# Kernel tuning notes

Hardware: AMD Instinct MI355X
Metric: run time of the kernel (lower is better)

The kernel has to match this reference:

```python
import jax, jax.numpy as jnp
import numpy as np

GROUPS = [16, 16, 32, 64, 192]
B, H, W = 8, 64, 64


def _shift(x, dy, dx):
    # out[i, j] = x[i - dy, j - dx], zero padded (equiv. of PoolConv's depthwise shift convs)
    Hh, Ww = x.shape[-2], x.shape[-1]
    pt, pb = max(dy, 0), max(-dy, 0)
    pl, pr = max(dx, 0), max(-dx, 0)
    xp = jnp.pad(x, ((0, 0), (0, 0), (pt, pb), (pl, pr)))
    return xp[..., pb:pb + Hh, pr:pr + Ww]


def _conv5(x, w, b):
    out = jax.lax.conv_general_dilated(x, w, (1, 1), ((2, 2), (2, 2)),
                                       dimension_numbers=("NCHW", "OIHW", "NCHW"))
    return out + b[None, :, None, None]


def _fill_pool(x, m1):
    # bottom: w[0,0]=1, pad 1 -> shift down-right; top: w[2,0]=1 -> shift up-right; right: w[2,0] of 5x5, pad 2 -> shift right by 2
    xm = x * m1
    return x + _shift(xm, 1, 1) + _shift(xm, -1, 1) + _shift(xm, 0, 2)


def _forward(y, mask, sws, sbs, cws, cbs):
    m0, m1 = mask[0], mask[1]
    starts = np.cumsum([0] + GROUPS[:-1])
    outs = []
    prev = None
    for i, g in enumerate(GROUPS):
        s = y[:, int(starts[i]):int(starts[i]) + g]
        anchor = _fill_pool(s * m0, m1)
        sp = _conv5(anchor, sws[i], sbs[i]) * (1.0 - m0)
        if i == 0:
            outs.append(sp)
            prev = s
        else:
            ch = _conv5(prev, cws[i - 1], cbs[i - 1])
            outs.append(sp)
            outs.append(ch)
            prev = jnp.concatenate([prev, s], axis=1)
    return tuple(outs)


def setup_inputs() -> dict:
    key = jax.random.key(0)
    ks = jax.random.split(key, 32)
    y = jax.random.normal(ks[0], (B, sum(GROUPS), H, W), jnp.float32)
    hh, ww = jnp.meshgrid(jnp.arange(H), jnp.arange(W), indexing="ij")
    m0 = (((hh + ww) % 2) == 0).astype(jnp.float32)[None, None]  # checkerboard anchor mask
    mask = jnp.stack([m0, 1.0 - m0], axis=0)  # [2,1,1,H,W]
    starts = np.cumsum([0] + GROUPS[:-1])
    inp = {"y": y, "mask": mask, "stage": 1}
    for i, g in enumerate(GROUPS):
        inp[f"sw{i}"] = 0.02 * jax.random.normal(ks[1 + i], (2 * g, g, 5, 5), jnp.float32)
        inp[f"sb{i}"] = jnp.zeros((2 * g,), jnp.float32)
    for i in range(1, len(GROUPS)):
        inp[f"cw{i}"] = 0.02 * jax.random.normal(ks[10 + i], (2 * GROUPS[i], int(starts[i]), 5, 5), jnp.float32)
        inp[f"cb{i}"] = jnp.zeros((2 * GROUPS[i],), jnp.float32)
    return inp


def reference(y, mask, stage, sw0, sb0, sw1, sb1, sw2, sb2, sw3, sb3, sw4, sb4,
              cw1, cb1, cw2, cb2, cw3, cb3, cw4, cb4):
    # stage != TRAIN branch: AdaptiveContext returns only the conv output
    return _forward(y, mask,
                    [sw0, sw1, sw2, sw3, sw4], [sb0, sb1, sb2, sb3, sb4],
                    [cw1, cw2, cw3, cw4], [cb1, cb2, cb3, cb4])
```

## Files before the change

kernel.cpp:

```cpp
#include <hip/hip_runtime.h>

typedef __bf16 bf16_t;
typedef __bf16 bf16x8 __attribute__((ext_vector_type(8)));
typedef float f32x16 __attribute__((ext_vector_type(16)));
typedef unsigned int u32;

#define CTOT 320
#define NPIX 32768

__device__ __forceinline__ void gload16(const void* g, void* l) {
  __builtin_amdgcn_global_load_lds((const __attribute__((address_space(1))) u32*)g,
                                   (__attribute__((address_space(3))) u32*)l, 16, 0, 0);
}

__device__ __forceinline__ void sync_drain(bool wait) {
  if (wait) asm volatile("s_waitcnt vmcnt(0)" ::: "memory");
  __builtin_amdgcn_sched_barrier(0);
  __builtin_amdgcn_s_barrier();
  __builtin_amdgcn_sched_barrier(0);
}

struct PrepParams {
  const float* y;
  bf16_t *yt, *ytp, *wt;
  const float* w[9];
  int IC[9], OC[9], OCp[9], wtoff[9], jst[9];
  uint4* zp;
};

__global__ __launch_bounds__(256) void k_prep(PrepParams Q) {
  int blk = blockIdx.x, tid = threadIdx.x;
  if (blk >= 2560) {
    int wb = blk - 2560;
    if (wb >= 572) { if (tid < 64) Q.zp[tid] = uint4{0u, 0u, 0u, 0u}; return; }
    int ci = 0;
#pragma unroll
    for (int i = 1; i < 9; ++i) if (wb >= Q.jst[i]) ci = i;
    int IC = Q.IC[ci], OCp = Q.OCp[ci], OC = Q.OC[ci];
    int idx = (wb - Q.jst[ci]) * 256 + tid;
    if (idx >= OCp * IC) return;
    int oc = idx / IC, ic = idx - oc * IC;
    bool valid = (oc < OC);
    const float* src = Q.w[ci] + (size_t)(oc * IC + ic) * 25;
    bf16_t* dst = Q.wt + Q.wtoff[ci];
    int icg = ic >> 3, ie = ic & 7;
#pragma unroll
    for (int t = 0; t < 25; ++t) {
      float v = valid ? src[t] : 0.0f;
      dst[(size_t)((t * (IC >> 3) + icg) * OCp + oc) * 8 + ie] = (bf16_t)v;
    }
    return;
  }
  __shared__ bf16_t T[64][72];
  int c0 = (blk % 5) * 64;
  int bh = blk / 5;
  int b = bh >> 6, h = bh & 63;
  {
    int c = tid >> 2, w0 = (tid & 3) << 4;
    const float* src = Q.y + (size_t)(b * CTOT + c0 + c) * 4096 + (h << 6) + w0;
#pragma unroll
    for (int j = 0; j < 16; j += 4) {
      float4 v = *(const float4*)(src + j);
      T[c][w0 + j + 0] = (bf16_t)v.x;
      T[c][w0 + j + 1] = (bf16_t)v.y;
      T[c][w0 + j + 2] = (bf16_t)v.z;
      T[c][w0 + j + 3] = (bf16_t)v.w;
    }
  }
  __syncthreads();
  {
    int w = tid >> 2, cq = (tid & 3) << 4;
    union { uint4 v; bf16_t b[8]; } u0, u1;
#pragma unroll
    for (int j = 0; j < 8; ++j) { u0.b[j] = T[cq + j][w]; u1.b[j] = T[cq + 8 + j][w]; }
    bf16_t* dst = Q.yt + (size_t)((bh << 6) | w) * CTOT + c0 + cq;
    *(uint4*)dst = u0.v;
    *(uint4*)(dst + 8) = u1.v;
  }
  if (tid < 128) {
    int j = tid >> 2, cq = (tid & 3) << 4;
    int w = (j << 1) + (h & 1);
    union { uint4 v; bf16_t b[8]; } u0, u1;
#pragma unroll
    for (int k = 0; k < 8; ++k) { u0.b[k] = T[cq + k][w]; u1.b[k] = T[cq + 8 + k][w]; }
    bf16_t* dst = Q.ytp + (size_t)((bh << 5) + j) * CTOT + c0 + cq;
    *(uint4*)dst = u0.v;
    *(uint4*)(dst + 8) = u1.v;
  }
}

struct ConvDesc {
  const float* bias;
  int out_off, wt_off;
  int IC, OC, OCp, chs, masked, job_start;
};
struct MainParams {
  const bf16_t* yt;
  const bf16_t* ytp;
  const bf16_t* wt;
  const bf16_t* zp;
  float* out;
  ConvDesc cv[9];
};

template <bool MASKED>
__device__ __forceinline__ void conv_run(const ConvDesc cd, const MainParams& P,
                                         int local, bf16_t* S) {
  constexpr int COLS = MASKED ? 36 : 68;
  constexpr int REAL = MASKED ? 720 : 816;
  constexpr int NSG  = MASKED ? 12 : 13;
  constexpr int SPL  = NSG * 512;
  constexpr int SINB = 2 * SPL;
  constexpr int SWO  = 2 * SINB;

  int mb = MASKED ? (local >> 5) : (local >> 6);
  int nb = local & (MASKED ? 31 : 63);
  int b  = MASKED ? (nb >> 2) : (nb >> 3);
  int hblk = MASKED ? ((nb & 3) << 4) : ((nb & 7) << 3);
  int tid = threadIdx.x, lane = tid & 63, wid = tid >> 6;
  int l31 = lane & 31, kq = lane >> 5;
  bool sin_role = (wid < 4);

  int octmax = (cd.OC - (mb << 6)) >> 5; if (octmax > 2) octmax = 2;

  f32x16 acc00 = {}, acc01 = {}, acc10 = {}, acc11 = {};

  int aofs = SWO + kq * 512 + l31 * 8;
  int bofs = kq * SPL + (MASKED ? (((wid << 1) * 36 + 1 + l31) * 8)
                                : ((wid * 68 + l31) * 8));

  const bf16_t* wtc = P.wt + cd.wt_off;
  int icgs = cd.IC >> 3;
  int nchunks = cd.IC >> 4;

  auto stage_sin = [&](int cb, int buf) {
    int ic0 = cb << 4;
    for (int g = wid; g < 2 * NSG; g += 4) {
      int p = (g >= NSG) ? 1 : 0;
      int gi = g - p * NSG;
      int s = (gi << 6) + lane;
      int rr = s / COLS, cc = s - rr * COLS;
      int h = hblk + rr - 2;
      const bf16_t* gp;
      if (!MASKED) {
        int w = cc - 2;
        bool inb = (s < REAL) && ((unsigned)h < 64u) && ((unsigned)w < 64u);
        gp = inb ? (P.yt + (size_t)((((b << 6) + (h & 63)) << 6) | (w & 63)) * CTOT
                        + cd.chs + ic0 + (p << 3))
                 : P.zp;
      } else {
        int j = cc - 1;
        bool inb = (s < REAL) && ((unsigned)h < 64u) && ((unsigned)j < 32u);
        gp = inb ? (P.ytp + (size_t)((((b << 6) + (h & 63)) << 5) + (j & 31)) * CTOT
                         + cd.chs + ic0 + (p << 3))
                 : P.zp;
      }
      gload16(gp, S + buf * SINB + p * SPL + (gi << 9));
    }
  };
  auto stage_sw = [&](int gstart, int gcnt, int swb, int cb) {
    int ic0 = cb << 4;
    for (int t = wid - 4; t < 2 * gcnt; t += 4) {
      int slot = t >> 1, icg = t & 1;
      int ti = gstart + slot;
      int tap = MASKED ? (2 * ti + 1) : ti;
      const bf16_t* gp = wtc +
          (size_t)((tap * icgs + (ic0 >> 3) + icg) * cd.OCp + (mb << 6) + lane) * 8;
      gload16(gp, S + SWO + ((swb * 7 + slot) << 10) + (icg << 9));
    }
  };

#define TAP_ONE(TI, SL)                                                         \
    {                                                                           \
      int tap_ = MASKED ? (2 * (TI) + 1) : (TI);                                \
      int dy_ = tap_ / 5, dx_ = tap_ % 5;                                       \
      bf16x8 af0 = *(const bf16x8*)(S + aofs + (SL) * 1024);                    \
      bf16x8 bf0, bf1;                                                          \
      if (!MASKED) {                                                            \
        int toff_ = (dy_ * 68 + dx_) * 8;                                       \
        bf0 = *(const bf16x8*)(Sn + bofs + toff_);                              \
        bf1 = *(const bf16x8*)(Sn + bofs + toff_ + 256);                        \
      } else {                                                                  \
        int j0_ = (dx_ - 1 - (dy_ & 1)) / 2;                                    \
        int j1_ = (dx_ - 2 - ((dy_ + 1) & 1)) / 2;                              \
        bf0 = *(const bf16x8*)(Sn + bofs + (dy_ * 36 + j0_) * 8);               \
        bf1 = *(const bf16x8*)(Sn + bofs + ((dy_ + 1) * 36 + j1_) * 8);         \
      }                                                                         \
      acc00 = __builtin_amdgcn_mfma_f32_32x32x16_bf16(af0, bf0, acc00, 0, 0, 0);\
      acc01 = __builtin_amdgcn_mfma_f32_32x32x16_bf16(af0, bf1, acc01, 0, 0, 0);\
      if (octmax > 1) {                                                         \
        bf16x8 af1 = *(const bf16x8*)(S + aofs + (SL) * 1024 + 256);            \
        acc10 = __builtin_amdgcn_mfma_f32_32x32x16_bf16(af1, bf0, acc10, 0,0,0);\
        acc11 = __builtin_amdgcn_mfma_f32_32x32x16_bf16(af1, bf1, acc11, 0,0,0);\
      }                                                                         \
    }
#define RUNG(GS, SB, CNT)                                                       \
    __builtin_amdgcn_s_setprio(1);                                              \
    _Pragma("unroll")                                                           \
    for (int s_ = 0; s_ < (CNT); ++s_) TAP_ONE((GS) + s_, (SB) + s_)            \
    __builtin_amdgcn_s_setprio(0);

  if (sin_role) stage_sin(0, 0);
  else          stage_sw(0, MASKED ? 6 : 7, 0, 0);

  for (int cb = 0; cb < nchunks; ++cb) {
    const bf16_t* Sn = S + (cb & 1) * SINB;
    sync_drain(true);
    if (sin_role) {
      if (cb + 1 < nchunks) stage_sin(cb + 1, (cb + 1) & 1);
    }
    if (!MASKED) {
      if (!sin_role) stage_sw(7, 6, 1, cb);
      RUNG(0, 0, 7)
      sync_drain(!sin_role);
      if (!sin_role) stage_sw(13, 6, 0, cb);
      RUNG(7, 7, 6)
      sync_drain(!sin_role);
      if (!sin_role) stage_sw(19, 6, 1, cb);
      RUNG(13, 0, 6)
      sync_drain(!sin_role);
      if (!sin_role && cb + 1 < nchunks) stage_sw(0, 7, 0, cb + 1);
      RUNG(19, 7, 6)
    } else {
      if (!sin_role) stage_sw(6, 6, 1, cb);
      RUNG(0, 0, 6)
      sync_drain(!sin_role);
      if (!sin_role && cb + 1 < nchunks) stage_sw(0, 6, 0, cb + 1);
      RUNG(6, 7, 6)
    }
  }
#undef RUNG
#undef TAP_ONE

  float* outp = P.out + cd.out_off;
#define EPI_U(A, OT, PT)                                                        \
  {                                                                             \
    int h = hblk + wid;                                                         \
    _Pragma("unroll")                                                           \
    for (int r = 0; r < 16; ++r) {                                              \
      int row = (r & 3) + ((r >> 2) << 3) + (kq << 2);                          \
      int oc = (mb << 6) + ((OT) << 5) + row;                                   \
      outp[(size_t)(b * cd.OC + oc) * 4096 + (h << 6) + ((PT) << 5) + l31] =    \
          (A)[r] + cd.bias[oc];                                                 \
    }                                                                           \
  }
#define EPI_M(A, OT, PT)                                                        \
  {                                                                             \
    int h = hblk + (wid << 1) + (PT);                                           \
    _Pragma("unroll")                                                           \
    for (int r = 0; r < 16; ++r) {                                              \
      int row = (r & 3) + ((r >> 2) << 3) + (kq << 2);                          \
      int oc = (mb << 6) + ((OT) << 5) + row;                                   \
      float val = (A)[r] + cd.bias[oc];                                         \
      float2 pr;                                                                \
      if ((PT) == 0) { pr.x = 0.0f; pr.y = val; }                               \
      else           { pr.x = val;  pr.y = 0.0f; }                              \
      *(float2*)(outp + (size_t)(b * cd.OC + oc) * 4096 + (h << 6) + (l31 << 1)) = pr; \
    }                                                                           \
  }
  if (!MASKED) {
    EPI_U(acc00, 0, 0); EPI_U(acc01, 0, 1);
    if (octmax > 1) { EPI_U(acc10, 1, 0); EPI_U(acc11, 1, 1); }
  } else {
    EPI_M(acc00, 0, 0); EPI_M(acc01, 0, 1);
    if (octmax > 1) { EPI_M(acc10, 1, 0); EPI_M(acc11, 1, 1); }
  }
#undef EPI_U
#undef EPI_M
}

__global__ __launch_bounds__(512, 4) void k_conv_main(MainParams P) {
  __shared__ bf16_t S[40960];
  int bid = blockIdx.x;
  int ci = 0;
#pragma unroll
  for (int i = 1; i < 9; ++i) if (bid >= P.cv[i].job_start) ci = i;
  ConvDesc cd = P.cv[ci];
  int local = bid - cd.job_start;
  if (cd.masked) conv_run<true>(cd, P, local, S);
  else           conv_run<false>(cd, P, local, S);
}

extern "C" void kernel_launch(void* const* d_in, const int* in_sizes, int n_in,
                              void* d_out, int out_size, void* d_ws, size_t ws_size,
                              hipStream_t stream) {
  const float* y = (const float*)d_in[0];
  bf16_t* yt  = (bf16_t*)d_ws;
  bf16_t* ytp = yt + (size_t)NPIX * CTOT;
  bf16_t* wt  = ytp + (size_t)(NPIX / 2) * CTOT;
  bf16_t* zp  = wt + 3660800;

  static const int ICv[9]  = {128,    192,    64,     32,     16,     64,     32,     16,    16};
  static const int OCv[9]  = {384,    384,    128,    64,     32,     128,    64,     32,    32};
  static const int OCp[9]  = {384,    384,    128,    64,     64,     128,    64,     64,    64};
  static const int WIDX[9] = {19,     11,     17,     15,     13,     9,      7,      5,     3};
  static const int BIDX[9] = {20,     12,     18,     16,     14,     10,     8,      6,     4};
  static const int CHS[9]  = {0,      128,    0,      0,      0,      64,     32,     16,    0};
  static const int MSK[9]  = {0,      1,      0,      0,      0,      1,      1,      1,     1};
  static const int WTOFF[9] = {0, 1228800, 3072000, 3276800, 3328000,
                               3353600, 3558400, 3609600, 3635200};
  static const int OUTOFF[9] = {28311552, 15728640, 11534336, 5242880, 2097152,
                                7340032,  3145728,  1048576,  0};
  static const int JOBST[9] = {0, 384, 576, 704, 768, 832, 896, 928, 960};
  static const int PJST[9] = {0, 192, 480, 512, 520, 524, 556, 564, 568};

  PrepParams Q;
  Q.y = y; Q.yt = yt; Q.ytp = ytp; Q.wt = wt; Q.zp = (uint4*)zp;
  for (int i = 0; i < 9; ++i) {
    Q.w[i] = (const float*)d_in[WIDX[i]];
    Q.IC[i] = ICv[i]; Q.OC[i] = OCv[i]; Q.OCp[i] = OCp[i];
    Q.wtoff[i] = WTOFF[i]; Q.jst[i] = PJST[i];
  }
  k_prep<<<3133, 256, 0, stream>>>(Q);

  MainParams P;
  P.yt = yt; P.ytp = ytp; P.wt = wt; P.zp = zp; P.out = (float*)d_out;
  for (int i = 0; i < 9; ++i) {
    P.cv[i].bias = (const float*)d_in[BIDX[i]];
    P.cv[i].out_off = OUTOFF[i];
    P.cv[i].wt_off = WTOFF[i];
    P.cv[i].IC = ICv[i]; P.cv[i].OC = OCv[i]; P.cv[i].OCp = OCp[i];
    P.cv[i].chs = CHS[i]; P.cv[i].masked = MSK[i];
    P.cv[i].job_start = JOBST[i];
  }
  k_conv_main<<<992, 512, 0, stream>>>(P);
}
```

Baseline: 157.7 us.

## Read conv weights directly from global and halve block tile size

Weight tiles are no longer staged into LDS by dedicated warps. Each wave now loads its A fragments straight from global memory (through the cache) per tap, so the warp-specialised producer/consumer split and its many barriers go away. Blocks shrink to 256 threads covering half as many rows, which doubles the grid and shrinks LDS use. The input-tile prefetch for the next chunk is issued partway through the tap loop. The cost is a global-load latency on every MFMA operand fetch and less reuse of each staged input tile.

```diff
diff --git a/kernel.cpp b/kernel.cpp
--- a/kernel.cpp
+++ b/kernel.cpp
@@ -11,13 +11,6 @@
 __device__ __forceinline__ void gload16(const void* g, void* l) {
   __builtin_amdgcn_global_load_lds((const __attribute__((address_space(1))) u32*)g,
                                    (__attribute__((address_space(3))) u32*)l, 16, 0, 0);
-}
-
-__device__ __forceinline__ void sync_drain(bool wait) {
-  if (wait) asm volatile("s_waitcnt vmcnt(0)" ::: "memory");
-  __builtin_amdgcn_sched_barrier(0);
-  __builtin_amdgcn_s_barrier();
-  __builtin_amdgcn_sched_barrier(0);
 }
 
 struct PrepParams {
@@ -106,32 +99,34 @@
 template <bool MASKED>
 __device__ __forceinline__ void conv_run(const ConvDesc cd, const MainParams& P,
                                          int local, bf16_t* S) {
+  constexpr int NT   = MASKED ? 12 : 25;
+  constexpr int P1   = MASKED ? 4 : 5;
   constexpr int COLS = MASKED ? 36 : 68;
-  constexpr int REAL = MASKED ? 720 : 816;
-  constexpr int NSG  = MASKED ? 12 : 13;
+  constexpr int REAL = MASKED ? 432 : 544;
+  constexpr int NSG  = MASKED ? 7 : 9;
   constexpr int SPL  = NSG * 512;
   constexpr int SINB = 2 * SPL;
-  constexpr int SWO  = 2 * SINB;
-
-  int mb = MASKED ? (local >> 5) : (local >> 6);
-  int nb = local & (MASKED ? 31 : 63);
-  int b  = MASKED ? (nb >> 2) : (nb >> 3);
-  int hblk = MASKED ? ((nb & 3) << 4) : ((nb & 7) << 3);
+
+  int mb = MASKED ? (local >> 6) : (local >> 7);
+  int nb = local & (MASKED ? 63 : 127);
+  int b  = MASKED ? (nb >> 3) : (nb >> 4);
+  int hblk = MASKED ? ((nb & 7) << 3) : ((nb & 15) << 2);
   int tid = threadIdx.x, lane = tid & 63, wid = tid >> 6;
   int l31 = lane & 31, kq = lane >> 5;
-  bool sin_role = (wid < 4);
 
   int octmax = (cd.OC - (mb << 6)) >> 5; if (octmax > 2) octmax = 2;
 
   f32x16 acc00 = {}, acc01 = {}, acc10 = {}, acc11 = {};
 
-  int aofs = SWO + kq * 512 + l31 * 8;
   int bofs = kq * SPL + (MASKED ? (((wid << 1) * 36 + 1 + l31) * 8)
                                 : ((wid * 68 + l31) * 8));
 
   const bf16_t* wtc = P.wt + cd.wt_off;
   int icgs = cd.IC >> 3;
   int nchunks = cd.IC >> 4;
+  size_t ocp8 = (size_t)cd.OCp << 3;
+  size_t wstride = (size_t)icgs * ocp8;
+  const bf16_t* wbase = wtc + (size_t)(kq * cd.OCp + (mb << 6) + l31) * 8;
 
   auto stage_sin = [&](int cb, int buf) {
     int ic0 = cb << 4;
@@ -158,23 +153,13 @@
       gload16(gp, S + buf * SINB + p * SPL + (gi << 9));
     }
   };
-  auto stage_sw = [&](int gstart, int gcnt, int swb, int cb) {
-    int ic0 = cb << 4;
-    for (int t = wid - 4; t < 2 * gcnt; t += 4) {
-      int slot = t >> 1, icg = t & 1;
-      int ti = gstart + slot;
-      int tap = MASKED ? (2 * ti + 1) : ti;
-      const bf16_t* gp = wtc +
-          (size_t)((tap * icgs + (ic0 >> 3) + icg) * cd.OCp + (mb << 6) + lane) * 8;
-      gload16(gp, S + SWO + ((swb * 7 + slot) << 10) + (icg << 9));
-    }
-  };
-
-#define TAP_ONE(TI, SL)                                                         \
+
+#define TAP_ONE(TI)                                                             \
     {                                                                           \
       int tap_ = MASKED ? (2 * (TI) + 1) : (TI);                                \
       int dy_ = tap_ / 5, dx_ = tap_ % 5;                                       \
-      bf16x8 af0 = *(const bf16x8*)(S + aofs + (SL) * 1024);                    \
+      const bf16_t* ap_ = wa + (size_t)tap_ * wstride;                          \
+      bf16x8 af0 = *(const bf16x8*)ap_;                                         \
       bf16x8 bf0, bf1;                                                          \
       if (!MASKED) {                                                            \
         int toff_ = (dy_ * 68 + dx_) * 8;                                       \
@@ -189,47 +174,32 @@
       acc00 = __builtin_amdgcn_mfma_f32_32x32x16_bf16(af0, bf0, acc00, 0, 0, 0);\
       acc01 = __builtin_amdgcn_mfma_f32_32x32x16_bf16(af0, bf1, acc01, 0, 0, 0);\
       if (octmax > 1) {                                                         \
-        bf16x8 af1 = *(const bf16x8*)(S + aofs + (SL) * 1024 + 256);            \
+        bf16x8 af1 = *(const bf16x8*)(ap_ + 256);                               \
         acc10 = __builtin_amdgcn_mfma_f32_32x32x16_bf16(af1, bf0, acc10, 0,0,0);\
         acc11 = __builtin_amdgcn_mfma_f32_32x32x16_bf16(af1, bf1, acc11, 0,0,0);\
       }                                                                         \
     }
-#define RUNG(GS, SB, CNT)                                                       \
-    __builtin_amdgcn_s_setprio(1);                                              \
-    _Pragma("unroll")                                                           \
-    for (int s_ = 0; s_ < (CNT); ++s_) TAP_ONE((GS) + s_, (SB) + s_)            \
-    __builtin_amdgcn_s_setprio(0);
-
-  if (sin_role) stage_sin(0, 0);
-  else          stage_sw(0, MASKED ? 6 : 7, 0, 0);
-
+
+  stage_sin(0, 0);
   for (int cb = 0; cb < nchunks; ++cb) {
     const bf16_t* Sn = S + (cb & 1) * SINB;
-    sync_drain(true);
-    if (sin_role) {
-      if (cb + 1 < nchunks) stage_sin(cb + 1, (cb + 1) & 1);
-    }
-    if (!MASKED) {
-      if (!sin_role) stage_sw(7, 6, 1, cb);
-      RUNG(0, 0, 7)
-      sync_drain(!sin_role);
-      if (!sin_role) stage_sw(13, 6, 0, cb);
-      RUNG(7, 7, 6)
-      sync_drain(!sin_role);
-      if (!sin_role) stage_sw(19, 6, 1, cb);
-      RUNG(13, 0, 6)
-      sync_drain(!sin_role);
-      if (!sin_role && cb + 1 < nchunks) stage_sw(0, 7, 0, cb + 1);
-      RUNG(19, 7, 6)
-    } else {
-      if (!sin_role) stage_sw(6, 6, 1, cb);
-      RUNG(0, 0, 6)
-      sync_drain(!sin_role);
-      if (!sin_role && cb + 1 < nchunks) stage_sw(0, 6, 0, cb + 1);
-      RUNG(6, 7, 6)
-    }
-  }
-#undef RUNG
+    const bf16_t* wa = wbase + (size_t)(cb << 1) * ocp8;
+    asm volatile("s_waitcnt vmcnt(0)" ::: "memory");
+    __builtin_amdgcn_sched_barrier(0);
+    __builtin_amdgcn_s_barrier();
+    __builtin_amdgcn_sched_barrier(0);
+    __builtin_amdgcn_s_setprio(1);
+#pragma unroll
+    for (int s_ = 0; s_ < P1; ++s_) TAP_ONE(s_)
+    __builtin_amdgcn_s_setprio(0);
+    __builtin_amdgcn_sched_barrier(0);
+    if (cb + 1 < nchunks) stage_sin(cb + 1, (cb + 1) & 1);
+    __builtin_amdgcn_sched_barrier(0);
+    __builtin_amdgcn_s_setprio(1);
+#pragma unroll
+    for (int s_ = P1; s_ < NT; ++s_) TAP_ONE(s_)
+    __builtin_amdgcn_s_setprio(0);
+  }
 #undef TAP_ONE
 
   float* outp = P.out + cd.out_off;
@@ -269,8 +239,8 @@
 #undef EPI_M
 }
 
-__global__ __launch_bounds__(512, 4) void k_conv_main(MainParams P) {
-  __shared__ bf16_t S[40960];
+__global__ __launch_bounds__(256, 3) void k_conv_main(MainParams P) {
+  __shared__ bf16_t S[18432];
   int bid = blockIdx.x;
   int ci = 0;
 #pragma unroll
@@ -301,7 +271,7 @@
                                3353600, 3558400, 3609600, 3635200};
   static const int OUTOFF[9] = {28311552, 15728640, 11534336, 5242880, 2097152,
                                 7340032,  3145728,  1048576,  0};
-  static const int JOBST[9] = {0, 384, 576, 704, 768, 832, 896, 928, 960};
+  static const int JOBST[9] = {0, 768, 1152, 1408, 1536, 1664, 1792, 1856, 1920};
   static const int PJST[9] = {0, 192, 480, 512, 520, 524, 556, 564, 568};
 
   PrepParams Q;
@@ -323,5 +293,5 @@
     P.cv[i].chs = CHS[i]; P.cv[i].masked = MSK[i];
     P.cv[i].job_start = JOBST[i];
   }
-  k_conv_main<<<992, 512, 0, stream>>>(P);
-}
+  k_conv_main<<<1984, 256, 0, stream>>>(P);
+}
```

After: 266.6 us. 1.69x slower.

## Drop warp specialization; use 4 compute waves each computing 4 pixel fragments

Applied to the files above, without the earlier changes.

Replaces the 8-wave block, split into 4 loader waves and 4 compute waves, with a 4-wave block where every wave both stages data and computes. Each wave now accumulates 4 N-fragments (two rows, or four masked rows) instead of 2, so each weight fragment read from LDS is reused across more MFMAs. Input staging for the next chunk moves to just before the last rung, and the custom drain barriers become plain __syncthreads. The trade-offs are more accumulator registers per wave (launch bounds 256,2) and less overlap between loads and compute, since there are no longer dedicated loader waves.

```diff
diff --git a/kernel.cpp b/kernel.cpp
--- a/kernel.cpp
+++ b/kernel.cpp
@@ -11,13 +11,6 @@
 __device__ __forceinline__ void gload16(const void* g, void* l) {
   __builtin_amdgcn_global_load_lds((const __attribute__((address_space(1))) u32*)g,
                                    (__attribute__((address_space(3))) u32*)l, 16, 0, 0);
-}
-
-__device__ __forceinline__ void sync_drain(bool wait) {
-  if (wait) asm volatile("s_waitcnt vmcnt(0)" ::: "memory");
-  __builtin_amdgcn_sched_barrier(0);
-  __builtin_amdgcn_s_barrier();
-  __builtin_amdgcn_sched_barrier(0);
 }
 
 struct PrepParams {
@@ -106,6 +99,7 @@
 template <bool MASKED>
 __device__ __forceinline__ void conv_run(const ConvDesc cd, const MainParams& P,
                                          int local, bf16_t* S) {
+  constexpr int NT   = MASKED ? 12 : 25;
   constexpr int COLS = MASKED ? 36 : 68;
   constexpr int REAL = MASKED ? 720 : 816;
   constexpr int NSG  = MASKED ? 12 : 13;
@@ -119,15 +113,14 @@
   int hblk = MASKED ? ((nb & 3) << 4) : ((nb & 7) << 3);
   int tid = threadIdx.x, lane = tid & 63, wid = tid >> 6;
   int l31 = lane & 31, kq = lane >> 5;
-  bool sin_role = (wid < 4);
 
   int octmax = (cd.OC - (mb << 6)) >> 5; if (octmax > 2) octmax = 2;
 
-  f32x16 acc00 = {}, acc01 = {}, acc10 = {}, acc11 = {};
+  f32x16 acc0[4] = {}, acc1[4] = {};
 
   int aofs = SWO + kq * 512 + l31 * 8;
-  int bofs = kq * SPL + (MASKED ? (((wid << 1) * 36 + 1 + l31) * 8)
-                                : ((wid * 68 + l31) * 8));
+  int bofs = kq * SPL + (MASKED ? (((wid << 2) * 36 + 1 + l31) * 8)
+                                : (((wid << 1) * 68 + l31) * 8));
 
   const bf16_t* wtc = P.wt + cd.wt_off;
   int icgs = cd.IC >> 3;
@@ -160,7 +153,7 @@
   };
   auto stage_sw = [&](int gstart, int gcnt, int swb, int cb) {
     int ic0 = cb << 4;
-    for (int t = wid - 4; t < 2 * gcnt; t += 4) {
+    for (int t = wid; t < 2 * gcnt; t += 4) {
       int slot = t >> 1, icg = t & 1;
       int ti = gstart + slot;
       int tap = MASKED ? (2 * ti + 1) : ti;
@@ -174,24 +167,24 @@
     {                                                                           \
       int tap_ = MASKED ? (2 * (TI) + 1) : (TI);                                \
       int dy_ = tap_ / 5, dx_ = tap_ % 5;                                       \
-      bf16x8 af0 = *(const bf16x8*)(S + aofs + (SL) * 1024);                    \
-      bf16x8 bf0, bf1;                                                          \
-      if (!MASKED) {                                                            \
-        int toff_ = (dy_ * 68 + dx_) * 8;                                       \
-        bf0 = *(const bf16x8*)(Sn + bofs + toff_);                              \
-        bf1 = *(const bf16x8*)(Sn + bofs + toff_ + 256);                        \
-      } else {                                                                  \
-        int j0_ = (dx_ - 1 - (dy_ & 1)) / 2;                                    \
-        int j1_ = (dx_ - 2 - ((dy_ + 1) & 1)) / 2;                              \
-        bf0 = *(const bf16x8*)(Sn + bofs + (dy_ * 36 + j0_) * 8);               \
-        bf1 = *(const bf16x8*)(Sn + bofs + ((dy_ + 1) * 36 + j1_) * 8);         \
-      }                                                                         \
-      acc00 = __builtin_amdgcn_mfma_f32_32x32x16_bf16(af0, bf0, acc00, 0, 0, 0);\
-      acc01 = __builtin_amdgcn_mfma_f32_32x32x16_bf16(af0, bf1, acc01, 0, 0, 0);\
-      if (octmax > 1) {                                                         \
-        bf16x8 af1 = *(const bf16x8*)(S + aofs + (SL) * 1024 + 256);            \
-        acc10 = __builtin_amdgcn_mfma_f32_32x32x16_bf16(af1, bf0, acc10, 0,0,0);\
-        acc11 = __builtin_amdgcn_mfma_f32_32x32x16_bf16(af1, bf1, acc11, 0,0,0);\
+      const bf16_t* sw_ = S + aofs + (SL) * 1024;                               \
+      bf16x8 af0 = *(const bf16x8*)sw_;                                         \
+      bf16x8 af1 = {};                                                          \
+      if (octmax > 1) af1 = *(const bf16x8*)(sw_ + 256);                        \
+      _Pragma("unroll")                                                         \
+      for (int nf = 0; nf < 4; ++nf) {                                          \
+        int ro_;                                                                \
+        if (!MASKED) {                                                          \
+          ro_ = ((((nf >> 1) + dy_) * 68) + ((nf & 1) << 5) + dx_) * 8;         \
+        } else {                                                                \
+          int joff_ = ((nf & 1) == 0) ? (dx_ - 1 - (dy_ & 1)) / 2               \
+                                      : (dx_ - 2 - ((dy_ + 1) & 1)) / 2;        \
+          ro_ = ((nf + dy_) * 36 + joff_) * 8;                                  \
+        }                                                                       \
+        bf16x8 bv = *(const bf16x8*)(Sn + bofs + ro_);                          \
+        acc0[nf] = __builtin_amdgcn_mfma_f32_32x32x16_bf16(af0, bv, acc0[nf], 0, 0, 0); \
+        if (octmax > 1)                                                         \
+          acc1[nf] = __builtin_amdgcn_mfma_f32_32x32x16_bf16(af1, bv, acc1[nf], 0, 0, 0); \
       }                                                                         \
     }
 #define RUNG(GS, SB, CNT)                                                       \
@@ -200,32 +193,34 @@
     for (int s_ = 0; s_ < (CNT); ++s_) TAP_ONE((GS) + s_, (SB) + s_)            \
     __builtin_amdgcn_s_setprio(0);
 
-  if (sin_role) stage_sin(0, 0);
-  else          stage_sw(0, MASKED ? 6 : 7, 0, 0);
-
+  stage_sin(0, 0);
+  stage_sw(0, MASKED ? 6 : 7, 0, 0);
   for (int cb = 0; cb < nchunks; ++cb) {
     const bf16_t* Sn = S + (cb & 1) * SINB;
-    sync_drain(true);
-    if (sin_role) {
-      if (cb + 1 < nchunks) stage_sin(cb + 1, (cb + 1) & 1);
-    }
+    __syncthreads();
     if (!MASKED) {
-      if (!sin_role) stage_sw(7, 6, 1, cb);
+      stage_sw(7, 6, 1, cb);
       RUNG(0, 0, 7)
-      sync_drain(!sin_role);
-      if (!sin_role) stage_sw(13, 6, 0, cb);
+      __syncthreads();
+      stage_sw(13, 6, 0, cb);
       RUNG(7, 7, 6)
-      sync_drain(!sin_role);
-      if (!sin_role) stage_sw(19, 6, 1, cb);
+      __syncthreads();
+      stage_sw(19, 6, 1, cb);
       RUNG(13, 0, 6)
-      sync_drain(!sin_role);
-      if (!sin_role && cb + 1 < nchunks) stage_sw(0, 7, 0, cb + 1);
+      __syncthreads();
+      if (cb + 1 < nchunks) {
+        stage_sin(cb + 1, (cb + 1) & 1);
+        stage_sw(0, 7, 0, cb + 1);
+      }
       RUNG(19, 7, 6)
     } else {
-      if (!sin_role) stage_sw(6, 6, 1, cb);
+      stage_sw(6, 6, 1, cb);
       RUNG(0, 0, 6)
-      sync_drain(!sin_role);
-      if (!sin_role && cb + 1 < nchunks) stage_sw(0, 6, 0, cb + 1);
+      __syncthreads();
+      if (cb + 1 < nchunks) {
+        stage_sin(cb + 1, (cb + 1) & 1);
+        stage_sw(0, 6, 0, cb + 1);
+      }
       RUNG(6, 7, 6)
     }
   }
@@ -233,44 +228,52 @@
 #undef TAP_ONE
 
   float* outp = P.out + cd.out_off;
-#define EPI_U(A, OT, PT)                                                        \
+#define EPI_U(A, OT, NF)                                                        \
   {                                                                             \
-    int h = hblk + wid;                                                         \
+    int h = hblk + (wid << 1) + ((NF) >> 1);                                    \
+    int wc = (((NF) & 1) << 5) + l31;                                           \
     _Pragma("unroll")                                                           \
     for (int r = 0; r < 16; ++r) {                                              \
       int row = (r & 3) + ((r >> 2) << 3) + (kq << 2);                          \
       int oc = (mb << 6) + ((OT) << 5) + row;                                   \
-      outp[(size_t)(b * cd.OC + oc) * 4096 + (h << 6) + ((PT) << 5) + l31] =    \
-          (A)[r] + cd.bias[oc];                                                 \
+      outp[(size_t)(b * cd.OC + oc) * 4096 + (h << 6) + wc] = (A)[r] + cd.bias[oc]; \
     }                                                                           \
   }
-#define EPI_M(A, OT, PT)                                                        \
+#define EPI_M(A, OT, NF)                                                        \
   {                                                                             \
-    int h = hblk + (wid << 1) + (PT);                                           \
+    int h = hblk + (wid << 2) + (NF);                                           \
     _Pragma("unroll")                                                           \
     for (int r = 0; r < 16; ++r) {                                              \
       int row = (r & 3) + ((r >> 2) << 3) + (kq << 2);                          \
       int oc = (mb << 6) + ((OT) << 5) + row;                                   \
       float val = (A)[r] + cd.bias[oc];                                         \
       float2 pr;                                                                \
-      if ((PT) == 0) { pr.x = 0.0f; pr.y = val; }                               \
-      else           { pr.x = val;  pr.y = 0.0f; }                              \
+      if (((NF) & 1) == 0) { pr.x = 0.0f; pr.y = val; }                         \
+      else                 { pr.x = val;  pr.y = 0.0f; }                        \
       *(float2*)(outp + (size_t)(b * cd.OC + oc) * 4096 + (h << 6) + (l31 << 1)) = pr; \
     }                                                                           \
   }
   if (!MASKED) {
-    EPI_U(acc00, 0, 0); EPI_U(acc01, 0, 1);
-    if (octmax > 1) { EPI_U(acc10, 1, 0); EPI_U(acc11, 1, 1); }
+#pragma unroll
+    for (int nf = 0; nf < 4; ++nf) EPI_U(acc0[nf], 0, nf)
+    if (octmax > 1) {
+#pragma unroll
+      for (int nf = 0; nf < 4; ++nf) EPI_U(acc1[nf], 1, nf)
+    }
   } else {
-    EPI_M(acc00, 0, 0); EPI_M(acc01, 0, 1);
-    if (octmax > 1) { EPI_M(acc10, 1, 0); EPI_M(acc11, 1, 1); }
+#pragma unroll
+    for (int nf = 0; nf < 4; ++nf) EPI_M(acc0[nf], 0, nf)
+    if (octmax > 1) {
+#pragma unroll
+      for (int nf = 0; nf < 4; ++nf) EPI_M(acc1[nf], 1, nf)
+    }
   }
 #undef EPI_U
 #undef EPI_M
 }
 
-__global__ __launch_bounds__(512, 4) void k_conv_main(MainParams P) {
-  __shared__ bf16_t S[40960];
+__global__ __launch_bounds__(256, 2) void k_conv_main(MainParams P) {
+  __shared__ bf16_t S[39936];
   int bid = blockIdx.x;
   int ci = 0;
 #pragma unroll
@@ -323,5 +326,5 @@
     P.cv[i].chs = CHS[i]; P.cv[i].masked = MSK[i];
     P.cv[i].job_start = JOBST[i];
   }
-  k_conv_main<<<992, 512, 0, stream>>>(P);
-}
+  k_conv_main<<<992, 256, 0, stream>>>(P);
+}
```

Measured after the change: 173.9 us. 10.3% more time.

## Replace two-buffer weight staging with triple-buffered 4-tap groups and partial vmcnt waits

Applied to the files above, without the earlier changes.

Weight tiles move from two large 6-7 tap buffers to a rotating three-slot ring of 4-tap groups, each prefetched two groups ahead across chunk boundaries. Weight loaders wait with vmcnt(2) instead of draining all loads, so outstanding loads stay in flight across barriers. LDS use shrinks a little. In exchange there are more barriers per chunk (7 for unmasked, 3 for masked), and some redundant clamped loads for the last group.

```diff
diff --git a/kernel.cpp b/kernel.cpp
--- a/kernel.cpp
+++ b/kernel.cpp
@@ -11,13 +11,6 @@
 __device__ __forceinline__ void gload16(const void* g, void* l) {
   __builtin_amdgcn_global_load_lds((const __attribute__((address_space(1))) u32*)g,
                                    (__attribute__((address_space(3))) u32*)l, 16, 0, 0);
-}
-
-__device__ __forceinline__ void sync_drain(bool wait) {
-  if (wait) asm volatile("s_waitcnt vmcnt(0)" ::: "memory");
-  __builtin_amdgcn_sched_barrier(0);
-  __builtin_amdgcn_s_barrier();
-  __builtin_amdgcn_sched_barrier(0);
 }
 
 struct PrepParams {
@@ -106,6 +99,8 @@
 template <bool MASKED>
 __device__ __forceinline__ void conv_run(const ConvDesc cd, const MainParams& P,
                                          int local, bf16_t* S) {
+  constexpr int NT   = MASKED ? 12 : 25;
+  constexpr int NG   = MASKED ? 3 : 7;
   constexpr int COLS = MASKED ? 36 : 68;
   constexpr int REAL = MASKED ? 720 : 816;
   constexpr int NSG  = MASKED ? 12 : 13;
@@ -125,7 +120,7 @@
 
   f32x16 acc00 = {}, acc01 = {}, acc10 = {}, acc11 = {};
 
-  int aofs = SWO + kq * 512 + l31 * 8;
+  int swoc = SWO + kq * 512 + l31 * 8;
   int bofs = kq * SPL + (MASKED ? (((wid << 1) * 36 + 1 + l31) * 8)
                                 : ((wid * 68 + l31) * 8));
 
@@ -158,15 +153,18 @@
       gload16(gp, S + buf * SINB + p * SPL + (gi << 9));
     }
   };
-  auto stage_sw = [&](int gstart, int gcnt, int swb, int cb) {
-    int ic0 = cb << 4;
-    for (int t = wid - 4; t < 2 * gcnt; t += 4) {
-      int slot = t >> 1, icg = t & 1;
-      int ti = gstart + slot;
+  auto stage_sw = [&](int cbn, int jn, int wbase) {
+    int ic0 = cbn << 4;
+    int t = wid - 4;
+#pragma unroll
+    for (int o2 = 0; o2 < 2; ++o2) {
+      int o = t + o2 * 4;
+      int slot = o >> 1, icg = o & 1;
+      int ti = 4 * jn + slot; if (ti >= NT) ti = NT - 1;
       int tap = MASKED ? (2 * ti + 1) : ti;
       const bf16_t* gp = wtc +
           (size_t)((tap * icgs + (ic0 >> 3) + icg) * cd.OCp + (mb << 6) + lane) * 8;
-      gload16(gp, S + SWO + ((swb * 7 + slot) << 10) + (icg << 9));
+      gload16(gp, S + SWO + wbase + (slot << 10) + (icg << 9));
     }
   };
 
@@ -174,7 +172,7 @@
     {                                                                           \
       int tap_ = MASKED ? (2 * (TI) + 1) : (TI);                                \
       int dy_ = tap_ / 5, dx_ = tap_ % 5;                                       \
-      bf16x8 af0 = *(const bf16x8*)(S + aofs + (SL) * 1024);                    \
+      bf16x8 af0 = *(const bf16x8*)(swp + (SL) * 1024);                         \
       bf16x8 bf0, bf1;                                                          \
       if (!MASKED) {                                                            \
         int toff_ = (dy_ * 68 + dx_) * 8;                                       \
@@ -189,47 +187,48 @@
       acc00 = __builtin_amdgcn_mfma_f32_32x32x16_bf16(af0, bf0, acc00, 0, 0, 0);\
       acc01 = __builtin_amdgcn_mfma_f32_32x32x16_bf16(af0, bf1, acc01, 0, 0, 0);\
       if (octmax > 1) {                                                         \
-        bf16x8 af1 = *(const bf16x8*)(S + aofs + (SL) * 1024 + 256);            \
+        bf16x8 af1 = *(const bf16x8*)(swp + (SL) * 1024 + 256);                 \
         acc10 = __builtin_amdgcn_mfma_f32_32x32x16_bf16(af1, bf0, acc10, 0,0,0);\
         acc11 = __builtin_amdgcn_mfma_f32_32x32x16_bf16(af1, bf1, acc11, 0,0,0);\
       }                                                                         \
     }
-#define RUNG(GS, SB, CNT)                                                       \
-    __builtin_amdgcn_s_setprio(1);                                              \
-    _Pragma("unroll")                                                           \
-    for (int s_ = 0; s_ < (CNT); ++s_) TAP_ONE((GS) + s_, (SB) + s_)            \
-    __builtin_amdgcn_s_setprio(0);
 
   if (sin_role) stage_sin(0, 0);
-  else          stage_sw(0, MASKED ? 6 : 7, 0, 0);
+  else { stage_sw(0, 0, 0); stage_sw(0, 1, 4096); }
+  int gcnt = 2, jN = 2, cbN = 0;
+  if (jN >= NG) { jN -= NG; ++cbN; }
+  int swW = 8192, swR = 0;
+  int totG = nchunks * NG;
 
   for (int cb = 0; cb < nchunks; ++cb) {
     const bf16_t* Sn = S + (cb & 1) * SINB;
-    sync_drain(true);
-    if (sin_role) {
-      if (cb + 1 < nchunks) stage_sin(cb + 1, (cb + 1) & 1);
-    }
-    if (!MASKED) {
-      if (!sin_role) stage_sw(7, 6, 1, cb);
-      RUNG(0, 0, 7)
-      sync_drain(!sin_role);
-      if (!sin_role) stage_sw(13, 6, 0, cb);
-      RUNG(7, 7, 6)
-      sync_drain(!sin_role);
-      if (!sin_role) stage_sw(19, 6, 1, cb);
-      RUNG(13, 0, 6)
-      sync_drain(!sin_role);
-      if (!sin_role && cb + 1 < nchunks) stage_sw(0, 7, 0, cb + 1);
-      RUNG(19, 7, 6)
-    } else {
-      if (!sin_role) stage_sw(6, 6, 1, cb);
-      RUNG(0, 0, 6)
-      sync_drain(!sin_role);
-      if (!sin_role && cb + 1 < nchunks) stage_sw(0, 6, 0, cb + 1);
-      RUNG(6, 7, 6)
-    }
-  }
-#undef RUNG
+#pragma unroll
+    for (int j = 0; j < NG; ++j) {
+      if (sin_role) {
+        if (j == 0) asm volatile("s_waitcnt vmcnt(0)" ::: "memory");
+      } else {
+        asm volatile("s_waitcnt vmcnt(2)" ::: "memory");
+      }
+      __builtin_amdgcn_sched_barrier(0);
+      __builtin_amdgcn_s_barrier();
+      __builtin_amdgcn_sched_barrier(0);
+      if (j == 0 && sin_role && cb + 1 < nchunks) stage_sin(cb + 1, (cb + 1) & 1);
+      if (!sin_role && gcnt < totG) stage_sw(cbN, jN, swW);
+      ++gcnt; if (++jN == NG) { jN = 0; ++cbN; }
+      swW = (swW == 8192) ? 0 : swW + 4096;
+
+      const bf16_t* swp = S + swoc + swR;
+      __builtin_amdgcn_s_setprio(1);
+      if (!MASKED && j == 6) {
+        TAP_ONE(24, 0)
+      } else {
+#pragma unroll
+        for (int s_ = 0; s_ < 4; ++s_) TAP_ONE(4 * j + s_, s_)
+      }
+      __builtin_amdgcn_s_setprio(0);
+      swR = (swR == 8192) ? 0 : swR + 4096;
+    }
+  }
 #undef TAP_ONE
 
   float* outp = P.out + cd.out_off;
@@ -270,7 +269,7 @@
 }
 
 __global__ __launch_bounds__(512, 4) void k_conv_main(MainParams P) {
-  __shared__ bf16_t S[40960];
+  __shared__ bf16_t S[38912];
   int bid = blockIdx.x;
   int ci = 0;
 #pragma unroll
```

Result: no change. 157.8 us (+0.1%).
